# Optimization experiments

Hardware: AMD Instinct MI355X
Metric: run time of the kernel (lower is better)

Reference implementation:

```python
import jax, jax.numpy as jnp
import numpy as np

B, T, C = 2, 2048, 1024
H = 16
D = C // H          # head_dim = 64
WIN = 256           # local window


def _rope(x):
    # x: [B, H, T, D]; rotate pairs (even, odd) with per-pair frequencies.
    t = x.shape[2]
    d = x.shape[-1] // 2
    theta = 10000.0 ** (-(jnp.arange(d, dtype=x.dtype) / d))          # [d]
    ang = jnp.arange(t, dtype=x.dtype)[:, None] * theta               # [T, d]
    sin, cos = jnp.sin(ang), jnp.cos(ang)                             # [T, d]
    x1, x2 = x[..., ::2], x[..., 1::2]                                # [B,H,T,d]
    out = jnp.stack([x1 * cos - x2 * sin, x1 * sin + x2 * cos], axis=-1)
    return out.reshape(x.shape)


def setup_inputs() -> dict:
    key = jax.random.key(0)
    k1, k2, k3 = jax.random.split(key, 3)
    s = 1.0 / np.sqrt(C)
    return {
        "x": jax.random.normal(k1, (B, T, C), dtype=jnp.float32),
        "w_qkv": jax.random.normal(k2, (3 * C, C), dtype=jnp.float32) * s,
        "w_out": jax.random.normal(k3, (C, C), dtype=jnp.float32) * s,
        "b_out": jnp.zeros((C,), dtype=jnp.float32),
    }


def reference(x, w_qkv, w_out, b_out):
    b, t, c = x.shape
    qkv = x @ w_qkv.T                                   # [B,T,3C]
    qkv = qkv.reshape(b, t, H, 3 * D).transpose(0, 2, 1, 3)  # [B,H,T,3D]
    q, k, v = jnp.split(qkv, 3, axis=-1)                # each [B,H,T,D]
    q, k = _rope(q), _rope(k)
    scores = jnp.einsum("bhqd,bhkd->bhqk", q, k) / jnp.sqrt(jnp.asarray(D, x.dtype))
    i = jnp.arange(t)[:, None]
    j = jnp.arange(t)[None, :]
    mask = (j <= i) & (j >= i - WIN)                    # causal local window
    scores = jnp.where(mask, scores, -jnp.inf)
    attn = jax.nn.softmax(scores, axis=-1)              # [B,H,T,T]
    out = jnp.einsum("bhqk,bhkd->bhqd", attn, v)        # [B,H,T,D]
    out = out.transpose(0, 2, 1, 3).reshape(b, t, c)    # [B,T,C]
    return out @ w_out.T + b_out
```

## Files before the change

### kernel.cpp

```cpp
#include <hip/hip_runtime.h>
#include <math.h>

#define BB 2
#define TT 2048
#define CC 1024
#define HH 16
#define DD 64
#define WINW 256

constexpr int MROWS  = BB * TT;
constexpr int NQKV   = 3 * CC;
constexpr int QKV_LD = 3 * CC;

typedef unsigned short ushort_t;
typedef __attribute__((ext_vector_type(8))) short  bf16x8;
typedef __attribute__((ext_vector_type(4))) float  f32x4;
typedef __attribute__((ext_vector_type(8))) unsigned short u16x8;

__device__ __forceinline__ float bf2f(ushort_t u) {
    return __uint_as_float(((unsigned int)u) << 16);
}
__device__ __forceinline__ ushort_t f2bf(float f) {
    unsigned int u = __float_as_uint(f);
    u += 0x7fffu + ((u >> 16) & 1u);
    return (ushort_t)(u >> 16);
}

__device__ __forceinline__ void async16(void* lds, const void* g) {
    __builtin_amdgcn_global_load_lds(
        (const __attribute__((address_space(1))) unsigned int*)g,
        (__attribute__((address_space(3))) unsigned int*)lds, 16, 0, 0);
}

#define ROPE_LN 0.2878231366242557f

constexpr int NX = MROWS * CC;
constexpr int NQ = NQKV * CC;
constexpr int NO = CC * CC;

__global__ __launch_bounds__(256)
void convert_all(const float* __restrict__ x, const float* __restrict__ wq,
                 const float* __restrict__ wo, ushort_t* __restrict__ xb,
                 ushort_t* __restrict__ wqb, ushort_t* __restrict__ wob) {
    int i = (blockIdx.x * 256 + threadIdx.x) * 4;
    const float* src;
    ushort_t* dst;
    if (i < NX)           { src = x  + i;             dst = xb  + i; }
    else if (i < NX + NQ) { src = wq + (i - NX);      dst = wqb + (i - NX); }
    else                  { src = wo + (i - NX - NQ); dst = wob + (i - NX - NQ); }
    float4 v = *(const float4*)src;
    ushort4 o;
    o.x = f2bf(v.x); o.y = f2bf(v.y); o.z = f2bf(v.z); o.w = f2bf(v.w);
    *(ushort4*)dst = o;
}

template <bool BIAS, bool OUT_BF16>
__global__ __launch_bounds__(256)
void gemm_nt_mfma(const ushort_t* __restrict__ A, const ushort_t* __restrict__ Bw,
                  const float* __restrict__ bias, void* __restrict__ Cc,
                  int M, int N, int K) {
    __shared__ __align__(16) ushort_t As[128 * 32];
    __shared__ __align__(16) ushort_t Bs[128 * 32];

    const int tid  = threadIdx.x;
    const int lane = tid & 63;
    const int wv   = tid >> 6;
    const int wr   = wv >> 1;
    const int wc   = wv & 1;
    const int bm   = blockIdx.y * 128;
    const int bn   = blockIdx.x * 128;

    const int srow = tid >> 2;
    const int scol = (tid & 3) * 8;

    const ushort_t* Ag = A + (size_t)(bm + srow) * K + scol;
    const ushort_t* Bg = Bw + (size_t)(bn + srow) * K + scol;

    f32x4 acc[4][4];
#pragma unroll
    for (int m = 0; m < 4; ++m)
#pragma unroll
        for (int n = 0; n < 4; ++n)
            acc[m][n] = f32x4{0.f, 0.f, 0.f, 0.f};

    const int fr = lane & 15;
    const int fq = lane >> 4;

    for (int k0 = 0; k0 < K; k0 += 32) {
        async16(&As[tid * 8],        Ag);
        async16(&As[2048 + tid * 8], Ag + (size_t)64 * K);
        async16(&Bs[tid * 8],        Bg);
        async16(&Bs[2048 + tid * 8], Bg + (size_t)64 * K);
        Ag += 32; Bg += 32;
        __syncthreads();

        bf16x8 af[4], bfv[4];
#pragma unroll
        for (int m = 0; m < 4; ++m)
            af[m] = *(const bf16x8*)&As[(wr * 64 + m * 16 + fr) * 32 + fq * 8];
#pragma unroll
        for (int n = 0; n < 4; ++n)
            bfv[n] = *(const bf16x8*)&Bs[(wc * 64 + n * 16 + fr) * 32 + fq * 8];
#pragma unroll
        for (int m = 0; m < 4; ++m)
#pragma unroll
            for (int n = 0; n < 4; ++n)
                acc[m][n] = __builtin_amdgcn_mfma_f32_16x16x32_bf16(
                    af[m], bfv[n], acc[m][n], 0, 0, 0);
        __syncthreads();
    }

#pragma unroll
    for (int m = 0; m < 4; ++m) {
#pragma unroll
        for (int n = 0; n < 4; ++n) {
            const int col = bn + wc * 64 + n * 16 + fr;
            const float bv = BIAS ? bias[col] : 0.0f;
#pragma unroll
            for (int j = 0; j < 4; ++j) {
                const int row = bm + wr * 64 + m * 16 + fq * 4 + j;
                float v = acc[m][n][j] + bv;
                if (OUT_BF16)
                    ((ushort_t*)Cc)[(size_t)row * N + col] = f2bf(v);
                else
                    ((float*)Cc)[(size_t)row * N + col] = v;
            }
        }
    }
}

#define MASKNEG (-1e30f)

__global__ __launch_bounds__(512)
void attn_mfma(const ushort_t* __restrict__ qkv, ushort_t* __restrict__ out) {
    __shared__ __align__(16) ushort_t Ks[2][64 * 64];
    __shared__ __align__(16) ushort_t Vlin[2][64 * 64];
    __shared__ __align__(16) ushort_t Vt[64 * 72];
    __shared__ __align__(16) ushort_t Ps[8][16 * 72];

    const int tid  = threadIdx.x;
    const int lane = tid & 63;
    const int w    = tid >> 6;
    const int fr   = lane & 15;
    const int fq   = lane >> 4;

    const int blk = blockIdx.x;
    const int qt  = blk & 15;
    const int h   = (blk >> 4) & 15;
    const int b   = blk >> 8;
    const int q0  = qt * 128;

    const ushort_t* base = qkv + (size_t)(b * TT) * QKV_LD + h * (3 * DD);

    const int srow = tid >> 3;
    const int cbs  = (tid & 7) ^ (srow & 7);

    float thK[4];
#pragma unroll
    for (int e = 0; e < 4; ++e)
        thK[e] = __expf(-ROPE_LN * (float)(cbs * 4 + e));

    bf16x8 qf0, qf1;
    {
        const int tq = q0 + w * 16 + fr;
        const ushort_t* qrow = base + (size_t)tq * QKV_LD;
        u16x8 r0 = *(const u16x8*)(qrow + fq * 8);
        u16x8 r1 = *(const u16x8*)(qrow + 32 + fq * 8);
        const float tf = (float)tq;
#pragma unroll
        for (int e = 0; e < 4; ++e) {
            float th0 = __expf(-ROPE_LN * (float)(fq * 4 + e));
            float a0 = tf * th0;
            float s0 = __sinf(a0), c0 = __cosf(a0);
            float x1 = bf2f(r0[2 * e]), x2 = bf2f(r0[2 * e + 1]);
            r0[2 * e]     = f2bf(x1 * c0 - x2 * s0);
            r0[2 * e + 1] = f2bf(x1 * s0 + x2 * c0);
            float th1 = __expf(-ROPE_LN * (float)(16 + fq * 4 + e));
            float a1 = tf * th1;
            float s1 = __sinf(a1), c1 = __cosf(a1);
            float y1 = bf2f(r1[2 * e]), y2 = bf2f(r1[2 * e + 1]);
            r1[2 * e]     = f2bf(y1 * c1 - y2 * s1);
            r1[2 * e + 1] = f2bf(y1 * s1 + y2 * c1);
        }
        qf0 = *(bf16x8*)&r0;
        qf1 = *(bf16x8*)&r1;
    }

    f32x4 oacc[4];
#pragma unroll
    for (int nd = 0; nd < 4; ++nd) oacc[nd] = f32x4{0.f, 0.f, 0.f, 0.f};
    float mj[4], lj[4];
#pragma unroll
    for (int j = 0; j < 4; ++j) { mj[j] = MASKNEG; lj[j] = 0.f; }

    const int kstart = (q0 >= WINW) ? (q0 - WINW) : 0;
    const int ntiles = (q0 + 128 - kstart) >> 6;

    {
        const ushort_t* src = base + (size_t)(kstart + srow) * QKV_LD + DD + cbs * 8;
        u16x8 kv = *(const u16x8*)src;
        const float tf = (float)(kstart + srow);
#pragma unroll
        for (int e = 0; e < 4; ++e) {
            float a = tf * thK[e];
            float s = __sinf(a), c = __cosf(a);
            float x1 = bf2f(kv[2 * e]), x2 = bf2f(kv[2 * e + 1]);
            kv[2 * e]     = f2bf(x1 * c - x2 * s);
            kv[2 * e + 1] = f2bf(x1 * s + x2 * c);
        }
        *(u16x8*)&Ks[0][tid * 8] = kv;
        async16(&Vlin[0][tid * 8], src + DD);
    }
    __syncthreads();

    int cur = 0;
    for (int t = 0; t < ntiles; ++t) {
        const int kt0 = kstart + t * 64;
        const bool pf = (t + 1 < ntiles);

        u16x8 kpre;
        if (pf) {
            const ushort_t* src =
                base + (size_t)(kt0 + 64 + srow) * QKV_LD + DD + cbs * 8;
            kpre = *(const u16x8*)src;
            async16(&Vlin[cur ^ 1][tid * 8], src + DD);
        }

        {
            u16x8 vv = *(const u16x8*)&Vlin[cur][lane * 64 + ((w ^ (lane & 7)) * 8)];
#pragma unroll
            for (int e = 0; e < 8; ++e)
                Vt[(w * 8 + e) * 72 + lane] = vv[e];
        }

        f32x4 s[4];
#pragma unroll
        for (int n = 0; n < 4; ++n) {
            const int krow = n * 16 + fr;
            bf16x8 kb0 = *(const bf16x8*)&Ks[cur][krow * 64 + ((fq ^ (krow & 7)) * 8)];
            bf16x8 kb1 = *(const bf16x8*)&Ks[cur][krow * 64 + (((fq + 4) ^ (krow & 7)) * 8)];
            f32x4 z = f32x4{0.f, 0.f, 0.f, 0.f};
            z = __builtin_amdgcn_mfma_f32_16x16x32_bf16(qf0, kb0, z, 0, 0, 0);
            s[n] = __builtin_amdgcn_mfma_f32_16x16x32_bf16(qf1, kb1, z, 0, 0, 0);
        }

        float pmax[4];
#pragma unroll
        for (int j = 0; j < 4; ++j) pmax[j] = MASKNEG;
#pragma unroll
        for (int n = 0; n < 4; ++n) {
            const int key = kt0 + n * 16 + fr;
#pragma unroll
            for (int j = 0; j < 4; ++j) {
                const int qi = q0 + w * 16 + fq * 4 + j;
                const bool ok = (key <= qi) && (key >= qi - WINW);
                float sv = ok ? s[n][j] * 0.125f : MASKNEG;
                s[n][j] = sv;
                pmax[j] = fmaxf(pmax[j], sv);
            }
        }
#pragma unroll
        for (int off = 1; off < 16; off <<= 1)
#pragma unroll
            for (int j = 0; j < 4; ++j)
                pmax[j] = fmaxf(pmax[j], __shfl_xor(pmax[j], off));

        float tl[4] = {0.f, 0.f, 0.f, 0.f};
#pragma unroll
        for (int j = 0; j < 4; ++j) {
            float mnew = fmaxf(mj[j], pmax[j]);
            float alpha = (mnew <= -1e29f) ? 1.0f : __expf(mj[j] - mnew);
            mj[j] = mnew;
            lj[j] *= alpha;
#pragma unroll
            for (int nd = 0; nd < 4; ++nd) oacc[nd][j] *= alpha;
        }
#pragma unroll
        for (int n = 0; n < 4; ++n) {
#pragma unroll
            for (int j = 0; j < 4; ++j) {
                float sv = s[n][j];
                float p = (sv <= -1e29f) ? 0.f : __expf(sv - mj[j]);
                tl[j] += p;
                Ps[w][(fq * 4 + j) * 72 + n * 16 + fr] = f2bf(p);
            }
        }
#pragma unroll
        for (int off = 1; off < 16; off <<= 1)
#pragma unroll
            for (int j = 0; j < 4; ++j)
                tl[j] += __shfl_xor(tl[j], off);
#pragma unroll
        for (int j = 0; j < 4; ++j) lj[j] += tl[j];

        if (pf) {
            const float tf = (float)(kt0 + 64 + srow);
#pragma unroll
            for (int e = 0; e < 4; ++e) {
                float a = tf * thK[e];
                float s2 = __sinf(a), c2 = __cosf(a);
                float x1 = bf2f(kpre[2 * e]), x2 = bf2f(kpre[2 * e + 1]);
                kpre[2 * e]     = f2bf(x1 * c2 - x2 * s2);
                kpre[2 * e + 1] = f2bf(x1 * s2 + x2 * c2);
            }
            *(u16x8*)&Ks[cur ^ 1][tid * 8] = kpre;
        }

        __syncthreads();

        bf16x8 pa0 = *(const bf16x8*)&Ps[w][fr * 72 + fq * 8];
        bf16x8 pa1 = *(const bf16x8*)&Ps[w][fr * 72 + 32 + fq * 8];
#pragma unroll
        for (int nd = 0; nd < 4; ++nd) {
            bf16x8 vb0 = *(const bf16x8*)&Vt[(nd * 16 + fr) * 72 + fq * 8];
            bf16x8 vb1 = *(const bf16x8*)&Vt[(nd * 16 + fr) * 72 + 32 + fq * 8];
            oacc[nd] = __builtin_amdgcn_mfma_f32_16x16x32_bf16(pa0, vb0, oacc[nd], 0, 0, 0);
            oacc[nd] = __builtin_amdgcn_mfma_f32_16x16x32_bf16(pa1, vb1, oacc[nd], 0, 0, 0);
        }

        __syncthreads();
        cur ^= 1;
    }

#pragma unroll
    for (int nd = 0; nd < 4; ++nd) {
#pragma unroll
        for (int j = 0; j < 4; ++j) {
            const int qi = q0 + w * 16 + fq * 4 + j;
            out[(size_t)(b * TT + qi) * CC + h * DD + nd * 16 + fr] =
                f2bf(oacc[nd][j] / lj[j]);
        }
    }
}

extern "C" void kernel_launch(void* const* d_in, const int* in_sizes, int n_in,
                              void* d_out, int out_size, void* d_ws, size_t ws_size,
                              hipStream_t stream) {
    const float* x     = (const float*)d_in[0];
    const float* w_qkv = (const float*)d_in[1];
    const float* w_out = (const float*)d_in[2];
    const float* b_out = (const float*)d_in[3];
    float* out = (float*)d_out;

    ushort_t* qkv_b  = (ushort_t*)d_ws;
    ushort_t* attn_b = qkv_b  + (size_t)MROWS * NQKV;
    ushort_t* xb     = attn_b + (size_t)MROWS * CC;
    ushort_t* wqb    = xb     + (size_t)MROWS * CC;
    ushort_t* wob    = wqb    + (size_t)NQKV * CC;

    convert_all<<<(NX + NQ + NO) / 1024, 256, 0, stream>>>(
        x, w_qkv, w_out, xb, wqb, wob);

    gemm_nt_mfma<false, true><<<dim3(NQKV / 128, MROWS / 128), 256, 0, stream>>>(
        xb, wqb, nullptr, qkv_b, MROWS, NQKV, CC);

    attn_mfma<<<BB * HH * (TT / 128), 512, 0, stream>>>(qkv_b, attn_b);

    gemm_nt_mfma<true, false><<<dim3(CC / 128, MROWS / 128), 256, 0, stream>>>(
        attn_b, wob, b_out, out, MROWS, CC, CC);
}
```

Measured before the change: 107.8 us.

## Replace QKV GEMM with 256x256-tile, 8-wave, phase-pipelined async-load kernel

Adds a dedicated QKV projection GEMM that uses 256x256 output tiles with 512 threads. It double-buffers shared memory with async global-to-LDS loads spread across four phases per K-step, swizzles the LDS layout to avoid bank conflicts, and raises MFMA priority with setprio. The aim is to overlap memory traffic with matrix-core work and cut global loads per FLOP. The trade-off is only 12x16=192 blocks, under one wave on a large GPU, plus more registers and LDS per block, which lowers occupancy. The epilogue also writes scalar bf16 stores that are not coalesced.

Result: no change. 105.8 us (-1.8%).

```diff
diff --git a/kernel.cpp b/kernel.cpp
--- a/kernel.cpp
+++ b/kernel.cpp
@@ -54,6 +54,115 @@
     *(ushort4*)dst = o;
 }
 
+__global__ __launch_bounds__(512)
+void gemm1_8phase(const ushort_t* __restrict__ A, const ushort_t* __restrict__ Bw,
+                  ushort_t* __restrict__ Cc) {
+    constexpr int K = 1024, N = 3072, NT = 16;
+    __shared__ __align__(16) ushort_t As[2][2][256 * 32];
+    __shared__ __align__(16) ushort_t Bs[2][2][256 * 32];
+
+    const int tid  = threadIdx.x;
+    const int lane = tid & 63;
+    const int w    = tid >> 6;
+    const int wm   = w >> 2;
+    const int wn   = w & 3;
+    const int fr   = lane & 15;
+    const int fq   = lane >> 4;
+    const int bm   = blockIdx.y * 256;
+    const int bn   = blockIdx.x * 256;
+
+    const int sr  = tid >> 2;
+    const int dcb = tid & 3;
+    const int scb = dcb ^ ((sr >> 1) & 3);
+
+    const int cbr = fq ^ ((fr >> 1) & 3);
+
+    f32x4 acc[8][4];
+#pragma unroll
+    for (int m = 0; m < 8; ++m)
+#pragma unroll
+        for (int n = 0; n < 4; ++n)
+            acc[m][n] = f32x4{0.f, 0.f, 0.f, 0.f};
+
+#pragma unroll
+    for (int p = 0; p < 4; ++p) {
+        const int skh = p >> 1;
+        const bool isB = p & 1;
+        const ushort_t* G = isB ? Bw : A;
+        const int br = isB ? bn : bm;
+        ushort_t* L = isB ? &Bs[0][skh][0] : &As[0][skh][0];
+#pragma unroll
+        for (int hh = 0; hh < 2; ++hh)
+            async16(&L[(hh * 128 + sr) * 32 + dcb * 8],
+                    G + (size_t)(br + hh * 128 + sr) * K + skh * 32 + scb * 8);
+    }
+
+    for (int t = 0; t < NT; ++t) {
+        const int d  = t & 1;
+        const int tn = (t + 1) & (NT - 1);
+        bf16x8 bfr[4];
+
+#pragma unroll
+        for (int ph = 0; ph < 4; ++ph) {
+            const int kh = ph >> 1;
+            const int mh = ph & 1;
+
+            {
+                const int skh = ph >> 1;
+                const bool isB = ph & 1;
+                const ushort_t* G = isB ? Bw : A;
+                const int br = isB ? bn : bm;
+                ushort_t* L = isB ? &Bs[d ^ 1][skh][0] : &As[d ^ 1][skh][0];
+#pragma unroll
+                for (int hh = 0; hh < 2; ++hh)
+                    async16(&L[(hh * 128 + sr) * 32 + dcb * 8],
+                            G + (size_t)(br + hh * 128 + sr) * K
+                              + (size_t)tn * 64 + skh * 32 + scb * 8);
+            }
+
+            if (mh == 0)
+                asm volatile("s_waitcnt vmcnt(6)" ::: "memory");
+            __builtin_amdgcn_s_barrier();
+            __builtin_amdgcn_sched_barrier(0);
+
+            if (mh == 0) {
+#pragma unroll
+                for (int n = 0; n < 4; ++n) {
+                    const int rb = wn * 64 + n * 16 + fr;
+                    bfr[n] = *(const bf16x8*)&Bs[d][kh][rb * 32 + cbr * 8];
+                }
+            }
+            bf16x8 afr[4];
+#pragma unroll
+            for (int i = 0; i < 4; ++i) {
+                const int ra = wm * 128 + (mh * 4 + i) * 16 + fr;
+                afr[i] = *(const bf16x8*)&As[d][kh][ra * 32 + cbr * 8];
+            }
+
+            __builtin_amdgcn_s_setprio(1);
+#pragma unroll
+            for (int i = 0; i < 4; ++i)
+#pragma unroll
+                for (int n = 0; n < 4; ++n)
+                    acc[mh * 4 + i][n] = __builtin_amdgcn_mfma_f32_16x16x32_bf16(
+                        afr[i], bfr[n], acc[mh * 4 + i][n], 0, 0, 0);
+            __builtin_amdgcn_s_setprio(0);
+            __builtin_amdgcn_sched_barrier(0);
+        }
+    }
+
+#pragma unroll
+    for (int m = 0; m < 8; ++m)
+#pragma unroll
+        for (int n = 0; n < 4; ++n)
+#pragma unroll
+            for (int j = 0; j < 4; ++j) {
+                const int row = bm + wm * 128 + m * 16 + fq * 4 + j;
+                const int col = bn + wn * 64 + n * 16 + fr;
+                Cc[(size_t)row * N + col] = f2bf(acc[m][n][j]);
+            }
+}
+
 template <bool BIAS, bool OUT_BF16>
 __global__ __launch_bounds__(256)
 void gemm_nt_mfma(const ushort_t* __restrict__ A, const ushort_t* __restrict__ Bw,
@@ -351,8 +460,8 @@
     convert_all<<<(NX + NQ + NO) / 1024, 256, 0, stream>>>(
         x, w_qkv, w_out, xb, wqb, wob);
 
-    gemm_nt_mfma<false, true><<<dim3(NQKV / 128, MROWS / 128), 256, 0, stream>>>(
-        xb, wqb, nullptr, qkv_b, MROWS, NQKV, CC);
+    gemm1_8phase<<<dim3(NQKV / 256, MROWS / 256), 512, 0, stream>>>(
+        xb, wqb, qkv_b);
 
     attn_mfma<<<BB * HH * (TT / 128), 512, 0, stream>>>(qkv_b, attn_b);
 
```
